# Kernel tuning notes

Hardware: AMD Instinct MI355X
Metric: run time of the kernel (lower is better)

The kernel has to match this reference:

```python
import jax, jax.numpy as jnp
import numpy as np

B, L = 4096, 256
LINK_DIM, LINK_EMB, SIG_EMB = 5, 8, 8
COMB = LINK_EMB + SIG_EMB  # 16


def _mlp3(x, w1, b1, w2, b2, w3, b3):
    h = jax.nn.relu(x @ w1 + b1)
    h = jax.nn.relu(h @ w2 + b2)
    return h @ w3 + b3


def setup_inputs() -> dict:
    key = jax.random.key(0)
    ks = jax.random.split(key, 20)
    f32 = jnp.float32

    def glorot(k, shape):
        fan_in = shape[0]
        return jax.random.normal(k, shape, dtype=f32) * (1.0 / np.sqrt(fan_in))

    inp = {
        "link_features": jax.random.normal(ks[0], (B, L, LINK_DIM), dtype=f32),
        "signal_state": jax.random.randint(ks[1], (B, L), 0, 8),
        # link encoder: 5 -> 16 -> 8
        "le_w1": glorot(ks[2], (LINK_DIM, 16)), "le_b1": jnp.zeros((16,), f32),
        "le_w2": glorot(ks[3], (16, LINK_EMB)), "le_b2": jnp.zeros((LINK_EMB,), f32),
        # signal char embedding table (8 chars x 8 dim)
        "emb": jax.random.normal(ks[4], (8, SIG_EMB), dtype=f32),
        # link selector head: 16 -> 32 -> 16 -> 1
        "ls_w1": glorot(ks[5], (COMB, 32)), "ls_b1": jnp.zeros((32,), f32),
        "ls_w2": glorot(ks[6], (32, 16)), "ls_b2": jnp.zeros((16,), f32),
        "ls_w3": glorot(ks[7], (16, 1)), "ls_b3": jnp.zeros((1,), f32),
        # action selector head: 16 -> 32 -> 16 -> 2
        "as_w1": glorot(ks[8], (COMB, 32)), "as_b1": jnp.zeros((32,), f32),
        "as_w2": glorot(ks[9], (32, 16)), "as_b2": jnp.zeros((16,), f32),
        "as_w3": glorot(ks[10], (16, 2)), "as_b3": jnp.zeros((2,), f32),
    }
    return inp


def reference(link_features, signal_state,
              le_w1, le_b1, le_w2, le_b2, emb,
              ls_w1, ls_b1, ls_w2, ls_b2, ls_w3, ls_b3,
              as_w1, as_b1, as_w2, as_b2, as_w3, as_b3):
    # Link encoder: [B, L, 5] -> [B, L, 8]
    h = jax.nn.relu(link_features @ le_w1 + le_b1)
    link_emb = jax.nn.relu(h @ le_w2 + le_b2)
    # Signal state embedding lookup: [B, L] -> [B, L, 8]
    sig_emb = emb[signal_state]
    # Fused gather+concat (replaces the per-(b,l) python loop): [B, L, 16]
    comb = jnp.concatenate([link_emb, sig_emb], axis=-1)
    link_scores = _mlp3(comb, ls_w1, ls_b1, ls_w2, ls_b2, ls_w3, ls_b3).squeeze(-1)
    action_values = _mlp3(comb, as_w1, as_b1, as_w2, as_b2, as_w3, as_b3)
    return link_scores, action_values
```

## Files before the change

### kernel.cpp

```cpp
#include <hip/hip_runtime.h>


#define BL_TOTAL (4096 * 256)

typedef _Float16 half4   __attribute__((ext_vector_type(4)));
typedef _Float16 half8   __attribute__((ext_vector_type(8)));
typedef __fp16   fp16x2  __attribute__((ext_vector_type(2)));
typedef float    floatx4 __attribute__((ext_vector_type(4)));

#define MFMA16(A, B, C) __builtin_amdgcn_mfma_f32_16x16x16f16((A), (B), (C), 0, 0, 0)
#define MFMA32(A, B, C) __builtin_amdgcn_mfma_f32_16x16x32_f16((A), (B), (C), 0, 0, 0)

static __device__ __forceinline__ half4 relu_pack(floatx4 c) {
    fp16x2 lo = __builtin_amdgcn_cvt_pkrtz(c[0], c[1]);
    fp16x2 hi = __builtin_amdgcn_cvt_pkrtz(c[2], c[3]);
    half4 h;
    h[0] = (_Float16)lo[0]; h[1] = (_Float16)lo[1];
    h[2] = (_Float16)hi[0]; h[3] = (_Float16)hi[1];
    return __builtin_elementwise_max(h, (half4)(_Float16)0.0f);
}

static __device__ __forceinline__ half4 pack_rtz(float a, float b, float c, float d) {
    fp16x2 lo = __builtin_amdgcn_cvt_pkrtz(a, b);
    fp16x2 hi = __builtin_amdgcn_cvt_pkrtz(c, d);
    half4 r;
    r[0] = (_Float16)lo[0]; r[1] = (_Float16)lo[1];
    r[2] = (_Float16)hi[0]; r[3] = (_Float16)hi[1];
    return r;
}

static __device__ __forceinline__ half4 pack4_rne(float a, float b, float c, float d) {
    half4 r; r[0] = (_Float16)a; r[1] = (_Float16)b; r[2] = (_Float16)c; r[3] = (_Float16)d;
    return r;
}

static __device__ __forceinline__ half8 cat8(half4 x, half4 y) {
    half8 r;
    r[0] = x[0]; r[1] = x[1]; r[2] = x[2]; r[3] = x[3];
    r[4] = y[0]; r[5] = y[1]; r[6] = y[2]; r[7] = y[3];
    return r;
}

struct InPair {
    float a0, a1, a2, a3, b0, b1, b2, b3;
    int sA, sB;
};

static __device__ __forceinline__ InPair load_pair(
    const float* __restrict__ lf, const int* __restrict__ ss,
    int posA, int g)
{
    InPair r;
    r.a0 = r.a1 = r.a2 = r.a3 = 0.0f;
    r.b0 = r.b1 = r.b2 = r.b3 = 0.0f;
    const int posB = posA + 16;
    if (g == 0) {
        r.a0 = lf[posA * 5 + 0]; r.a1 = lf[posA * 5 + 1];
        r.a2 = lf[posA * 5 + 2]; r.a3 = lf[posA * 5 + 3];
        r.b0 = lf[posB * 5 + 0]; r.b1 = lf[posB * 5 + 1];
        r.b2 = lf[posB * 5 + 2]; r.b3 = lf[posB * 5 + 3];
    } else if (g == 1) {
        r.a0 = lf[posA * 5 + 4];
        r.b0 = lf[posB * 5 + 4];
    }
    r.sA = ss[posA];
    r.sB = ss[posB];
    return r;
}

__global__ __launch_bounds__(256, 4) void dqn_mfma(
    const float* __restrict__ lf,
    const int*   __restrict__ ss,
    const float* __restrict__ le_w1, const float* __restrict__ le_b1,
    const float* __restrict__ le_w2, const float* __restrict__ le_b2,
    const float* __restrict__ emb,
    const float* __restrict__ ls_w1, const float* __restrict__ ls_b1,
    const float* __restrict__ ls_w2, const float* __restrict__ ls_b2,
    const float* __restrict__ ls_w3, const float* __restrict__ ls_b3,
    const float* __restrict__ as_w1, const float* __restrict__ as_b1,
    const float* __restrict__ as_w2, const float* __restrict__ as_b2,
    const float* __restrict__ as_w3, const float* __restrict__ as_b3,
    float* __restrict__ out)
{
    const int lane = threadIdx.x & 63;
    const int wave = threadIdx.x >> 6;
    const int m16  = lane & 15;
    const int g    = lane >> 4;
    const int k0   = g * 4;

    const int tile0 = blockIdx.x * 32 + wave * 8;

    InPair p0 = load_pair(lf, ss, (tile0 + 0) * 16 + m16, g);
    InPair p1 = load_pair(lf, ss, (tile0 + 2) * 16 + m16, g);

    __shared__ half4    f4LDS[6][64];
    __shared__ half8    f8LDS[3][64];
    __shared__ floatx4  bLDS[9][64];
    __shared__ _Float16 embLDS[64];

    if (wave == 0) {
        f4LDS[0][lane] = pack4_rne(
            (k0 + 0 < 5) ? le_w1[(k0 + 0) * 16 + m16] : 0.0f,
            (k0 + 1 < 5) ? le_w1[(k0 + 1) * 16 + m16] : 0.0f,
            (k0 + 2 < 5) ? le_w1[(k0 + 2) * 16 + m16] : 0.0f,
            (k0 + 3 < 5) ? le_w1[(k0 + 3) * 16 + m16] : 0.0f);
        f4LDS[4][lane] = pack4_rne(as_w1[(k0+0)*32 + m16],      as_w1[(k0+1)*32 + m16],
                                   as_w1[(k0+2)*32 + m16],      as_w1[(k0+3)*32 + m16]);
        floatx4 b1, b3_2, b5;
        #pragma unroll
        for (int r = 0; r < 4; ++r) {
            b1[r]   = le_b1[4 * g + r];
            b3_2[r] = as_b1[4 * g + r];
            b5[r]   = 0.0f;
        }
        if (g == 0) { b5[0] = ls_b3[0]; b5[1] = as_b3[0]; b5[2] = as_b3[1]; }
        bLDS[0][lane] = b1;
        bLDS[4][lane] = b3_2;
        bLDS[8][lane] = b5;
    } else if (wave == 1) {
        f4LDS[1][lane] = pack4_rne(
            (m16 < 8) ? le_w2[(k0 + 0) * 8 + m16] : 0.0f,
            (m16 < 8) ? le_w2[(k0 + 1) * 8 + m16] : 0.0f,
            (m16 < 8) ? le_w2[(k0 + 2) * 8 + m16] : 0.0f,
            (m16 < 8) ? le_w2[(k0 + 3) * 8 + m16] : 0.0f);
        f4LDS[5][lane] = pack4_rne(as_w1[(k0+0)*32 + 16 + m16], as_w1[(k0+1)*32 + 16 + m16],
                                   as_w1[(k0+2)*32 + 16 + m16], as_w1[(k0+3)*32 + 16 + m16]);
        f8LDS[0][lane] = cat8(
            pack4_rne(ls_w2[(k0+0)*16 + m16],    ls_w2[(k0+1)*16 + m16],
                      ls_w2[(k0+2)*16 + m16],    ls_w2[(k0+3)*16 + m16]),
            pack4_rne(ls_w2[(16+k0+0)*16 + m16], ls_w2[(16+k0+1)*16 + m16],
                      ls_w2[(16+k0+2)*16 + m16], ls_w2[(16+k0+3)*16 + m16]));
        floatx4 b2, b3_3;
        #pragma unroll
        for (int r = 0; r < 4; ++r) {
            b2[r]   = (4 * g + r < 8) ? le_b2[4 * g + r] : 0.0f;
            b3_3[r] = as_b1[16 + 4 * g + r];
        }
        bLDS[1][lane] = b2;
        bLDS[5][lane] = b3_3;
    } else if (wave == 2) {
        f4LDS[2][lane] = pack4_rne(ls_w1[(k0+0)*32 + m16],      ls_w1[(k0+1)*32 + m16],
                                   ls_w1[(k0+2)*32 + m16],      ls_w1[(k0+3)*32 + m16]);
        f8LDS[1][lane] = cat8(
            pack4_rne(as_w2[(k0+0)*16 + m16],    as_w2[(k0+1)*16 + m16],
                      as_w2[(k0+2)*16 + m16],    as_w2[(k0+3)*16 + m16]),
            pack4_rne(as_w2[(16+k0+0)*16 + m16], as_w2[(16+k0+1)*16 + m16],
                      as_w2[(16+k0+2)*16 + m16], as_w2[(16+k0+3)*16 + m16]));
        floatx4 b3_0, b4ls;
        #pragma unroll
        for (int r = 0; r < 4; ++r) {
            b3_0[r] = ls_b1[4 * g + r];
            b4ls[r] = ls_b2[4 * g + r];
        }
        bLDS[2][lane] = b3_0;
        bLDS[6][lane] = b4ls;
    } else {
        f4LDS[3][lane] = pack4_rne(ls_w1[(k0+0)*32 + 16 + m16], ls_w1[(k0+1)*32 + 16 + m16],
                                   ls_w1[(k0+2)*32 + 16 + m16], ls_w1[(k0+3)*32 + 16 + m16]);
        f8LDS[2][lane] = cat8(
            pack4_rne(
                (m16 == 0) ? ls_w3[k0 + 0] : 0.0f,
                (m16 == 0) ? ls_w3[k0 + 1] : 0.0f,
                (m16 == 0) ? ls_w3[k0 + 2] : 0.0f,
                (m16 == 0) ? ls_w3[k0 + 3] : 0.0f),
            pack4_rne(
                (m16 == 1) ? as_w3[(k0+0)*2] : ((m16 == 2) ? as_w3[(k0+0)*2 + 1] : 0.0f),
                (m16 == 1) ? as_w3[(k0+1)*2] : ((m16 == 2) ? as_w3[(k0+1)*2 + 1] : 0.0f),
                (m16 == 1) ? as_w3[(k0+2)*2] : ((m16 == 2) ? as_w3[(k0+2)*2 + 1] : 0.0f),
                (m16 == 1) ? as_w3[(k0+3)*2] : ((m16 == 2) ? as_w3[(k0+3)*2 + 1] : 0.0f)));
        floatx4 b3_1, b4as;
        #pragma unroll
        for (int r = 0; r < 4; ++r) {
            b3_1[r] = ls_b1[16 + 4 * g + r];
            b4as[r] = as_b2[4 * g + r];
        }
        bLDS[3][lane] = b3_1;
        bLDS[7][lane] = b4as;
        embLDS[lane] = (_Float16)emb[lane];
    }
    __syncthreads();

    const half4 a1    = f4LDS[0][lane];
    const half4 a2    = f4LDS[1][lane];
    const half4 a3_0  = f4LDS[2][lane];
    const half4 a3_1  = f4LDS[3][lane];
    const half4 a3_2  = f4LDS[4][lane];
    const half4 a3_3  = f4LDS[5][lane];
    const half8 a4ls  = f8LDS[0][lane];
    const half8 a4as  = f8LDS[1][lane];
    const half8 a5    = f8LDS[2][lane];
    const floatx4 bias1   = bLDS[0][lane];
    const floatx4 bias2   = bLDS[1][lane];
    const floatx4 bias3_0 = bLDS[2][lane];
    const floatx4 bias3_1 = bLDS[3][lane];
    const floatx4 bias3_2 = bLDS[4][lane];
    const floatx4 bias3_3 = bLDS[5][lane];
    const floatx4 bias4ls = bLDS[6][lane];
    const floatx4 bias4as = bLDS[7][lane];
    const floatx4 bias5   = bLDS[8][lane];

    float* __restrict__ out2 = out + BL_TOTAL;

    #pragma unroll
    for (int t = 0; t < 8; t += 2) {
        InPair p2 = {};
        if (t + 4 < 8)
            p2 = load_pair(lf, ss, (tile0 + t + 4) * 16 + m16, g);

        const int posA = (tile0 + t) * 16 + m16;
        const int posB = posA + 16;

        half4 evA = *reinterpret_cast<const half4*>(&embLDS[p0.sA * 8 + (g & 1) * 4]);
        half4 evB = *reinterpret_cast<const half4*>(&embLDS[p0.sB * 8 + (g & 1) * 4]);

        half4 b1A = pack_rtz(p0.a0, p0.a1, p0.a2, p0.a3);
        half4 b1B = pack_rtz(p0.b0, p0.b1, p0.b2, p0.b3);

        floatx4 c1A = MFMA16(a1, b1A, bias1);
        floatx4 c1B = MFMA16(a1, b1B, bias1);
        half4 h1A = relu_pack(c1A);
        half4 h1B = relu_pack(c1B);

        floatx4 c2A = MFMA16(a2, h1A, bias2);
        floatx4 c2B = MFMA16(a2, h1B, bias2);
        half4 b3A = relu_pack(c2A);
        half4 b3B = relu_pack(c2B);
        if (g >= 2) { b3A = evA; b3B = evB; }

        floatx4 c30A = MFMA16(a3_0, b3A, bias3_0);
        floatx4 c30B = MFMA16(a3_0, b3B, bias3_0);
        floatx4 c31A = MFMA16(a3_1, b3A, bias3_1);
        floatx4 c31B = MFMA16(a3_1, b3B, bias3_1);
        floatx4 c32A = MFMA16(a3_2, b3A, bias3_2);
        floatx4 c32B = MFMA16(a3_2, b3B, bias3_2);
        floatx4 c33A = MFMA16(a3_3, b3A, bias3_3);
        floatx4 c33B = MFMA16(a3_3, b3B, bias3_3);
        half4 p0A = relu_pack(c30A), p1A = relu_pack(c31A);
        half4 p2A = relu_pack(c32A), p3A = relu_pack(c33A);
        half4 p0B = relu_pack(c30B), p1B = relu_pack(c31B);
        half4 p2B = relu_pack(c32B), p3B = relu_pack(c33B);

        floatx4 clsA = MFMA32(a4ls, cat8(p0A, p1A), bias4ls);
        floatx4 clsB = MFMA32(a4ls, cat8(p0B, p1B), bias4ls);
        floatx4 casA = MFMA32(a4as, cat8(p2A, p3A), bias4as);
        floatx4 casB = MFMA32(a4as, cat8(p2B, p3B), bias4as);
        half4 hlsA = relu_pack(clsA), hasA = relu_pack(casA);
        half4 hlsB = relu_pack(clsB), hasB = relu_pack(casB);

        floatx4 c5A = MFMA32(a5, cat8(hlsA, hasA), bias5);
        floatx4 c5B = MFMA32(a5, cat8(hlsB, hasB), bias5);

        if (g == 0) {
            out[posA] = c5A[0];
            out[posB] = c5B[0];
            reinterpret_cast<float2*>(out2)[posA] = make_float2(c5A[1], c5A[2]);
            reinterpret_cast<float2*>(out2)[posB] = make_float2(c5B[1], c5B[2]);
        }

        p0 = p1;
        p1 = p2;
    }
}

extern "C" void kernel_launch(void* const* d_in, const int* in_sizes, int n_in,
                              void* d_out, int out_size, void* d_ws, size_t ws_size,
                              hipStream_t stream) {
    const float* lf    = (const float*)d_in[0];
    const int*   ss    = (const int*)  d_in[1];
    const float* le_w1 = (const float*)d_in[2];
    const float* le_b1 = (const float*)d_in[3];
    const float* le_w2 = (const float*)d_in[4];
    const float* le_b2 = (const float*)d_in[5];
    const float* emb   = (const float*)d_in[6];
    const float* ls_w1 = (const float*)d_in[7];
    const float* ls_b1 = (const float*)d_in[8];
    const float* ls_w2 = (const float*)d_in[9];
    const float* ls_b2 = (const float*)d_in[10];
    const float* ls_w3 = (const float*)d_in[11];
    const float* ls_b3 = (const float*)d_in[12];
    const float* as_w1 = (const float*)d_in[13];
    const float* as_b1 = (const float*)d_in[14];
    const float* as_w2 = (const float*)d_in[15];
    const float* as_b2 = (const float*)d_in[16];
    const float* as_w3 = (const float*)d_in[17];
    const float* as_b3 = (const float*)d_in[18];
    float* out = (float*)d_out;

    dqn_mfma<<<2048, 256, 0, stream>>>(
        lf, ss, le_w1, le_b1, le_w2, le_b2, emb,
        ls_w1, ls_b1, ls_w2, ls_b2, ls_w3, ls_b3,
        as_w1, as_b1, as_w2, as_b2, as_w3, as_b3,
        out);
}
```

Baseline: 19.96 us.

## Stage per-wave link features and signals through LDS with coalesced vector loads

Each wave now loads its whole 128-position slice of link features and signal states up front with contiguous float4/float2/int4 loads. The slice is staged into a padded, stride-6 LDS region that aliases the weight/bias pool after those values are read into registers. The loop then reads inputs from LDS instead of doing strided scalar global loads with a two-deep register prefetch. This is meant to cut uncoalesced global traffic, at the cost of an extra block barrier and the LDS writes and reads.

```diff
diff --git a/kernel.cpp b/kernel.cpp
--- a/kernel.cpp
+++ b/kernel.cpp
@@ -41,30 +41,31 @@
     return r;
 }
 
-struct InPair {
+struct InP {
     float a0, a1, a2, a3, b0, b1, b2, b3;
     int sA, sB;
 };
 
-static __device__ __forceinline__ InPair load_pair(
-    const float* __restrict__ lf, const int* __restrict__ ss,
-    int posA, int g)
+static __device__ __forceinline__ InP read_in(
+    const float* __restrict__ lfS, const int* __restrict__ ssS,
+    int t, int m16, int g)
 {
-    InPair r;
+    InP r;
     r.a0 = r.a1 = r.a2 = r.a3 = 0.0f;
     r.b0 = r.b1 = r.b2 = r.b3 = 0.0f;
-    const int posB = posA + 16;
+    const int pA = t * 16 + m16;
+    const int pB = pA + 16;
     if (g == 0) {
-        r.a0 = lf[posA * 5 + 0]; r.a1 = lf[posA * 5 + 1];
-        r.a2 = lf[posA * 5 + 2]; r.a3 = lf[posA * 5 + 3];
-        r.b0 = lf[posB * 5 + 0]; r.b1 = lf[posB * 5 + 1];
-        r.b2 = lf[posB * 5 + 2]; r.b3 = lf[posB * 5 + 3];
+        const float* q = lfS + pA * 6;
+        r.a0 = q[0]; r.a1 = q[1]; r.a2 = q[2]; r.a3 = q[3];
+        const float* u = lfS + pB * 6;
+        r.b0 = u[0]; r.b1 = u[1]; r.b2 = u[2]; r.b3 = u[3];
     } else if (g == 1) {
-        r.a0 = lf[posA * 5 + 4];
-        r.b0 = lf[posB * 5 + 4];
+        r.a0 = lfS[pA * 6 + 4];
+        r.b0 = lfS[pB * 6 + 4];
     }
-    r.sA = ss[posA];
-    r.sB = ss[posB];
+    r.sA = ssS[pA];
+    r.sB = ssS[pB];
     return r;
 }
 
@@ -90,13 +91,19 @@
 
     const int tile0 = blockIdx.x * 32 + wave * 8;
 
-    InPair p0 = load_pair(lf, ss, (tile0 + 0) * 16 + m16, g);
-    InPair p1 = load_pair(lf, ss, (tile0 + 2) * 16 + m16, g);
-
-    __shared__ half4    f4LDS[6][64];
-    __shared__ half8    f8LDS[3][64];
-    __shared__ floatx4  bLDS[9][64];
+    const float* src = lf + (long)tile0 * 80;
+    float4 va = *reinterpret_cast<const float4*>(src + lane * 10);
+    float4 vb = *reinterpret_cast<const float4*>(src + lane * 10 + 4);
+    float2 vc = *reinterpret_cast<const float2*>(src + lane * 10 + 8);
+    int4 sv = make_int4(0, 0, 0, 0);
+    if (lane < 32)
+        sv = *reinterpret_cast<const int4*>(ss + tile0 * 16 + lane * 4);
+
+    __shared__ floatx4 poolRaw[960];
     __shared__ _Float16 embLDS[64];
+    half4   (*f4LDS)[64] = reinterpret_cast<half4 (*)[64]>(reinterpret_cast<char*>(poolRaw));
+    half8   (*f8LDS)[64] = reinterpret_cast<half8 (*)[64]>(reinterpret_cast<char*>(poolRaw) + 3072);
+    floatx4 (*bLDS)[64]  = reinterpret_cast<floatx4 (*)[64]>(reinterpret_cast<char*>(poolRaw) + 6144);
 
     if (wave == 0) {
         f4LDS[0][lane] = pack4_rne(
@@ -199,22 +206,37 @@
     const floatx4 bias4as = bLDS[7][lane];
     const floatx4 bias5   = bLDS[8][lane];
 
+    __syncthreads();
+
+    float* lfS = reinterpret_cast<float*>(reinterpret_cast<char*>(poolRaw) + wave * 3584);
+    int*   ssS = reinterpret_cast<int*>(reinterpret_cast<char*>(poolRaw) + wave * 3584 + 3072);
+
+    {
+        float* w0 = lfS + (2 * lane) * 6;
+        w0[0] = va.x; w0[1] = va.y; w0[2] = va.z; w0[3] = va.w; w0[4] = vb.x;
+        float* w1 = lfS + (2 * lane + 1) * 6;
+        w1[0] = vb.y; w1[1] = vb.z; w1[2] = vb.w; w1[3] = vc.x; w1[4] = vc.y;
+        if (lane < 32)
+            reinterpret_cast<int4*>(ssS)[lane] = sv;
+    }
+
     float* __restrict__ out2 = out + BL_TOTAL;
+
+    InP q0 = read_in(lfS, ssS, 0, m16, g);
 
     #pragma unroll
     for (int t = 0; t < 8; t += 2) {
-        InPair p2 = {};
-        if (t + 4 < 8)
-            p2 = load_pair(lf, ss, (tile0 + t + 4) * 16 + m16, g);
+        InP q1;
+        if (t + 2 < 8) q1 = read_in(lfS, ssS, t + 2, m16, g);
 
         const int posA = (tile0 + t) * 16 + m16;
         const int posB = posA + 16;
 
-        half4 evA = *reinterpret_cast<const half4*>(&embLDS[p0.sA * 8 + (g & 1) * 4]);
-        half4 evB = *reinterpret_cast<const half4*>(&embLDS[p0.sB * 8 + (g & 1) * 4]);
-
-        half4 b1A = pack_rtz(p0.a0, p0.a1, p0.a2, p0.a3);
-        half4 b1B = pack_rtz(p0.b0, p0.b1, p0.b2, p0.b3);
+        half4 evA = *reinterpret_cast<const half4*>(&embLDS[q0.sA * 8 + (g & 1) * 4]);
+        half4 evB = *reinterpret_cast<const half4*>(&embLDS[q0.sB * 8 + (g & 1) * 4]);
+
+        half4 b1A = pack_rtz(q0.a0, q0.a1, q0.a2, q0.a3);
+        half4 b1B = pack_rtz(q0.b0, q0.b1, q0.b2, q0.b3);
 
         floatx4 c1A = MFMA16(a1, b1A, bias1);
         floatx4 c1B = MFMA16(a1, b1B, bias1);
@@ -257,8 +279,7 @@
             reinterpret_cast<float2*>(out2)[posB] = make_float2(c5B[1], c5B[2]);
         }
 
-        p0 = p1;
-        p1 = p2;
+        q0 = q1;
     }
 }
 
```

Result: faster. 19.49 us (-2.4%).
